# Kernel optimization log

Measured on AMD Instinct MI355X. Metric: run time of the kernel, lower is better.

The kernel has to match this reference:

```python
import jax, jax.numpy as jnp
import numpy as np

L, B, Q, D = 6, 2, 300, 256  # levels, batch, num queries, embed dim


def setup_inputs() -> dict:
    key = jax.random.key(0)
    ks = jax.random.split(key, 20)
    s = 1.0 / np.sqrt(D)
    s2 = 1.0 / np.sqrt(2 * D)
    inp = {
        "hs": jax.random.normal(ks[0], (L, B, Q, D), jnp.float32),
        # per-level proj_q / proj_k (Linear(D, D) cloned L times)
        "Wq": jax.random.uniform(ks[1], (L, D, D), jnp.float32, -s, s),
        "bq": jax.random.uniform(ks[2], (L, D), jnp.float32, -s, s),
        "Wk": jax.random.uniform(ks[3], (L, D, D), jnp.float32, -s, s),
        "bk": jax.random.uniform(ks[4], (L, D), jnp.float32, -s, s),
        # final subject/object projections on hs[-1]
        "Wsub": jax.random.uniform(ks[5], (D, D), jnp.float32, -s, s),
        "bsub": jax.random.uniform(ks[6], (D,), jnp.float32, -s, s),
        "Wobj": jax.random.uniform(ks[7], (D, D), jnp.float32, -s, s),
        "bobj": jax.random.uniform(ks[8], (D,), jnp.float32, -s, s),
        # gate: Linear(2D, 1)
        "Wg": jax.random.uniform(ks[9], (2 * D, 1), jnp.float32, -s2, s2),
        "bg": jax.random.uniform(ks[10], (1,), jnp.float32, -s2, s2),
        # MLPHEAD: 2D -> D -> D -> 1
        "W1": jax.random.uniform(ks[11], (2 * D, D), jnp.float32, -s2, s2),
        "b1": jax.random.uniform(ks[12], (D,), jnp.float32, -s2, s2),
        "W2": jax.random.uniform(ks[13], (D, D), jnp.float32, -s, s),
        "b2": jax.random.uniform(ks[14], (D,), jnp.float32, -s, s),
        "W3": jax.random.uniform(ks[15], (D, 1), jnp.float32, -s, s),
        "b3": jax.random.uniform(ks[16], (1,), jnp.float32, -s, s),
    }
    return inp


def reference(hs, Wq, bq, Wk, bk, Wsub, bsub, Wobj, bobj, Wg, bg, W1, b1, W2, b2, W3, b3):
    l, b, q, d = hs.shape
    # per-level projections: [L, B, Q, D]
    Qs = jnp.einsum('lbqd,lde->lbqe', hs, Wq) + bq[:, None, None, :]
    Ks = jnp.einsum('lbqd,lde->lbqe', hs, Wk) + bk[:, None, None, :]
    # extra (L+1)-th level from final sub/obj projections of hs[-1]
    sub = hs[-1] @ Wsub + bsub  # [B, Q, D]
    obj = hs[-1] @ Wobj + bobj
    Q_all = jnp.concatenate([Qs, sub[None]], axis=0)  # [L+1, B, Q, D]
    K_all = jnp.concatenate([Ks, obj[None]], axis=0)
    # gate logit for pair (i, j) at level m = wa.q_m[i] + wb.k_m[j] + bg,
    # identical math to sigmoid(Linear(cat([q_i, k_j]))) without materializing
    # the [B, Q, Q, L+1, 2D] broadcast tensor.
    wa, wb = Wg[:d, 0], Wg[d:, 0]
    gq = jnp.einsum('lbqd,d->lbq', Q_all, wa)  # [L+1, B, Q]
    gk = jnp.einsum('lbqd,d->lbq', K_all, wb)
    gate = jax.nn.sigmoid(gq[:, :, :, None] + gk[:, :, None, :] + bg[0])  # [L+1, B, Qi, Qj]
    # gated sum over levels; query half depends on i, key half on j
    out_q = jnp.einsum('lbij,lbid->bijd', gate, Q_all)  # [B, Q, Q, D]
    out_k = jnp.einsum('lbij,lbjd->bijd', gate, K_all)
    gated = jnp.concatenate([out_q, out_k], axis=-1)  # [B, Q, Q, 2D]
    # rel predictor MLP: 2D -> D -> D -> 1
    x = jax.nn.relu(gated @ W1 + b1)
    x = jax.nn.relu(x @ W2 + b2)
    pred = (x @ W3 + b3)[..., 0]  # [B, Q, Q]
    pred_rel = jnp.broadcast_to(pred[None], (l,) + pred.shape)  # [L, B, Q, Q]
    return pred_rel
```

## Files before the change

### kernel.cpp

```cpp
#include <hip/hip_runtime.h>


typedef _Float16 half8 __attribute__((ext_vector_type(8)));
typedef float floatx4 __attribute__((ext_vector_type(4)));

#define MFMA16(a, b, c) __builtin_amdgcn_mfma_f32_16x16x32_f16((a), (b), (c), 0, 0, 0)

__global__ __launch_bounds__(256) void k_wprep(
    const float* __restrict__ Wq, const float* __restrict__ Wk,
    const float* __restrict__ Wsub, const float* __restrict__ Wobj,
    const float* __restrict__ W1, const float* __restrict__ W2,
    _Float16* __restrict__ WT)
{
    int eid = blockIdx.x * 256 + threadIdx.x;
    int mat = eid >> 13;
    int rem = eid & 8191;
    int tileid = rem >> 6;
    int lane = rem & 63;
    const float* src;
    if      (mat < 6)  src = Wq + mat * 65536;
    else if (mat < 12) src = Wk + (mat - 6) * 65536;
    else if (mat == 12) src = Wsub;
    else if (mat == 13) src = Wobj;
    else if (mat == 14) src = W1;
    else if (mat == 15) src = W1 + 65536;
    else               src = W2;
    int nb = tileid >> 3, kb = tileid & 7;
    int n = nb * 16 + (lane & 15);
    int k = kb * 32 + (lane >> 4) * 8;
    half8 h;
    #pragma unroll
    for (int j = 0; j < 8; ++j) h[j] = (_Float16)src[(k + j) * 256 + n];
    *(half8*)(WT + mat * 65536 + tileid * 512 + lane * 8) = h;
}

__global__ __launch_bounds__(256) void k_projpq(
    const float* __restrict__ hs, const _Float16* __restrict__ WT,
    const float* __restrict__ bq, const float* __restrict__ bk,
    const float* __restrict__ bsub, const float* __restrict__ bobj,
    const float* __restrict__ Wg,
    _Float16* __restrict__ PQt, _Float16* __restrict__ PKt,
    float* __restrict__ g_ws)
{
    __shared__ __align__(16) _Float16 Ah[64][264];
    __shared__ __align__(16) _Float16 X[64][264];

    int bid = blockIdx.x;
    int s = bid / 5, mt5 = bid - s * 5;
    int qk = s & 1, rr = s >> 1;
    int l = rr % 7, b = rr / 7;
    int hs_l = (l < 6) ? l : 5;
    const float* src = hs + (hs_l * 2 + b) * 76800;
    int projmat = (l < 6) ? (qk * 6 + l) : (12 + qk);
    const _Float16* WprojT = WT + projmat * 65536;
    const _Float16* W1hT   = WT + (14 + qk) * 65536;
    const float* bias = (l < 6) ? ((qk ? bk : bq) + l * 256) : (qk ? bobj : bsub);
    _Float16* dstP = qk ? PKt : PQt;
    const float* wvec = Wg + qk * 256;
    float* gdst = g_ws + qk * 4200 + (l * 2 + b) * 300;
    int m0 = mt5 * 64;

    int t = threadIdx.x, lane = t & 63, wv = t >> 6;
    int mr = lane & 15, hf = lane >> 4;

    {
        int row = t >> 2, qt = t & 3;
        int m = m0 + row; if (m > 299) m = 299;
        const float* p = src + m * 256 + qt * 64;
        #pragma unroll
        for (int i = 0; i < 16; ++i) {
            float4 v = *(const float4*)(p + 4 * i);
            _Float16* d = &Ah[row][qt * 64 + 4 * i];
            d[0] = (_Float16)v.x; d[1] = (_Float16)v.y;
            d[2] = (_Float16)v.z; d[3] = (_Float16)v.w;
        }
    }
    __syncthreads();

    floatx4 acc[4][4];
    #pragma unroll
    for (int i = 0; i < 4; ++i)
        #pragma unroll
        for (int j = 0; j < 4; ++j) acc[i][j] = floatx4{0.f, 0.f, 0.f, 0.f};
    for (int ks = 0; ks < 8; ++ks) {
        half8 afr[4];
        #pragma unroll
        for (int mt = 0; mt < 4; ++mt)
            afr[mt] = *(const half8*)&Ah[mt * 16 + mr][ks * 32 + hf * 8];
        #pragma unroll
        for (int nt = 0; nt < 4; ++nt) {
            half8 bfr = *(const half8*)(WprojT + (((wv * 4 + nt) * 8 + ks) << 9) + lane * 8);
            #pragma unroll
            for (int mt = 0; mt < 4; ++mt)
                acc[mt][nt] = MFMA16(afr[mt], bfr, acc[mt][nt]);
        }
    }

    #pragma unroll
    for (int nt = 0; nt < 4; ++nt) {
        int col = wv * 64 + nt * 16 + mr;
        float bb = bias[col];
        #pragma unroll
        for (int mt = 0; mt < 4; ++mt)
            #pragma unroll
            for (int r = 0; r < 4; ++r)
                X[mt * 16 + hf * 4 + r][col] = (_Float16)(acc[mt][nt][r] + bb);
    }
    __syncthreads();

    {
        int row = t >> 2, qt = t & 3;
        float sum = 0.f;
        #pragma unroll
        for (int i = 0; i < 64; i += 8) {
            half8 xv = *(const half8*)&X[row][qt * 64 + i];
            const float* wp = wvec + qt * 64 + i;
            float4 w0 = *(const float4*)wp;
            float4 w1 = *(const float4*)(wp + 4);
            sum += (float)xv[0] * w0.x + (float)xv[1] * w0.y
                 + (float)xv[2] * w0.z + (float)xv[3] * w0.w
                 + (float)xv[4] * w1.x + (float)xv[5] * w1.y
                 + (float)xv[6] * w1.z + (float)xv[7] * w1.w;
        }
        sum += __shfl_xor(sum, 1);
        sum += __shfl_xor(sum, 2);
        int m = m0 + row;
        if (qt == 0 && m < 300) gdst[m] = sum;
    }

    floatx4 acc2[4][4];
    #pragma unroll
    for (int i = 0; i < 4; ++i)
        #pragma unroll
        for (int j = 0; j < 4; ++j) acc2[i][j] = floatx4{0.f, 0.f, 0.f, 0.f};
    for (int ks = 0; ks < 8; ++ks) {
        half8 afr[4];
        #pragma unroll
        for (int mt = 0; mt < 4; ++mt)
            afr[mt] = *(const half8*)&X[mt * 16 + mr][ks * 32 + hf * 8];
        #pragma unroll
        for (int nt = 0; nt < 4; ++nt) {
            half8 bfr = *(const half8*)(W1hT + (((wv * 4 + nt) * 8 + ks) << 9) + lane * 8);
            #pragma unroll
            for (int mt = 0; mt < 4; ++mt)
                acc2[mt][nt] = MFMA16(afr[mt], bfr, acc2[mt][nt]);
        }
    }

    #pragma unroll
    for (int nt = 0; nt < 4; ++nt) {
        int n = wv * 64 + nt * 16 + mr;
        #pragma unroll
        for (int mt = 0; mt < 4; ++mt)
            #pragma unroll
            for (int r = 0; r < 4; ++r) {
                int m = m0 + mt * 16 + hf * 4 + r;
                if (m < 300)
                    dstP[((size_t)(b * 38 + (m >> 3)) * 256 + n) * 56 + l * 8 + (m & 7)] =
                        (_Float16)acc2[mt][nt][r];
            }
    }
}

__global__ __launch_bounds__(256, 4) void k_fused(
    const _Float16* __restrict__ PQt, const _Float16* __restrict__ PKt,
    const float* __restrict__ g_ws, const float* __restrict__ b1,
    const _Float16* __restrict__ W2T, const float* __restrict__ b2,
    const float* __restrict__ W3, const float* __restrict__ b3,
    const float* __restrict__ bg, float* __restrict__ out)
{
    union SM {
        _Float16 Pt[256][72];
        _Float16 X[64][264];
    };
    __shared__ __align__(16) SM sm;
    __shared__ float gate[7][64];

    int t = threadIdx.x, lane = t & 63, wv = t >> 6;
    int mr = lane & 15, hf = lane >> 4;
    int bid = blockIdx.x;
    int b = bid / 1444, rem = bid - b * 1444;
    int it = rem / 38, jt = rem - it * 38;
    int i0 = it * 8, j0 = jt * 8;

    float bg0 = bg[0];
    for (int task = t; task < 448; task += 256) {
        int l = task >> 6, row = task & 63;
        int i = i0 + (row >> 3); if (i > 299) i = 299;
        int j = j0 + (row & 7);  if (j > 299) j = 299;
        float z = g_ws[l * 600 + b * 300 + i] + g_ws[4200 + l * 600 + b * 300 + j] + bg0;
        gate[l][row] = 1.0f / (1.0f + expf(-z));
    }

    floatx4 acc1[4][4];
    #pragma unroll
    for (int i = 0; i < 4; ++i)
        #pragma unroll
        for (int j = 0; j < 4; ++j) acc1[i][j] = floatx4{0.f, 0.f, 0.f, 0.f};

    for (int pass = 0; pass < 2; ++pass) {
        const _Float16* src = pass ? PKt : PQt;
        int tb = pass ? jt : it;
        const _Float16* gp = src + ((size_t)(b * 38 + tb) * 256 + t) * 56;
        __syncthreads();
        #pragma unroll
        for (int l = 0; l < 7; ++l)
            *(half8*)&sm.Pt[t][l * 8] = *(const half8*)(gp + l * 8);
        *(half8*)&sm.Pt[t][56] = half8{};
        __syncthreads();

        #pragma unroll
        for (int ktl = 0; ktl < 2; ++ktl) {
            int l = ktl * 4 + hf;
            half8 afr[4];
            #pragma unroll
            for (int mt = 0; mt < 4; ++mt) {
                int r = mt * 16 + mr;
                float g = (l < 7) ? gate[l][r] : 0.f;
                _Float16 gh = (_Float16)g;
                int jstar = pass ? (r & 7) : (r >> 3);
                half8 f;
                #pragma unroll
                for (int j = 0; j < 8; ++j)
                    f[j] = (j == jstar) ? gh : (_Float16)0.f;
                afr[mt] = f;
            }
            #pragma unroll
            for (int nt = 0; nt < 4; ++nt) {
                half8 bfr = *(const half8*)&sm.Pt[wv * 64 + nt * 16 + mr][ktl * 32 + hf * 8];
                #pragma unroll
                for (int mt = 0; mt < 4; ++mt)
                    acc1[mt][nt] = MFMA16(afr[mt], bfr, acc1[mt][nt]);
            }
        }
    }
    __syncthreads();

    #pragma unroll
    for (int nt = 0; nt < 4; ++nt) {
        int col = wv * 64 + nt * 16 + mr;
        float bb = b1[col];
        #pragma unroll
        for (int mt = 0; mt < 4; ++mt)
            #pragma unroll
            for (int r = 0; r < 4; ++r) {
                float v = acc1[mt][nt][r] + bb;
                v = v > 0.f ? v : 0.f;
                sm.X[mt * 16 + hf * 4 + r][col] = (_Float16)v;
            }
    }
    __syncthreads();

    floatx4 acc2[4][4];
    #pragma unroll
    for (int i = 0; i < 4; ++i)
        #pragma unroll
        for (int j = 0; j < 4; ++j) acc2[i][j] = floatx4{0.f, 0.f, 0.f, 0.f};
    for (int s = 0; s < 8; ++s) {
        half8 afr[4];
        #pragma unroll
        for (int mt = 0; mt < 4; ++mt)
            afr[mt] = *(const half8*)&sm.X[mt * 16 + mr][s * 32 + hf * 8];
        #pragma unroll
        for (int nt = 0; nt < 4; ++nt) {
            half8 bfr = *(const half8*)(W2T + (((wv * 4 + nt) * 8 + s) << 9) + lane * 8);
            #pragma unroll
            for (int mt = 0; mt < 4; ++mt)
                acc2[mt][nt] = MFMA16(afr[mt], bfr, acc2[mt][nt]);
        }
    }
    __syncthreads();

    #pragma unroll
    for (int nt = 0; nt < 4; ++nt) {
        int col = wv * 64 + nt * 16 + mr;
        float bb = b2[col];
        #pragma unroll
        for (int mt = 0; mt < 4; ++mt)
            #pragma unroll
            for (int r = 0; r < 4; ++r) {
                float v = acc2[mt][nt][r] + bb;
                v = v > 0.f ? v : 0.f;
                sm.X[mt * 16 + hf * 4 + r][col] = (_Float16)v;
            }
    }
    __syncthreads();

    {
        int r = t >> 2, qd = t & 3;
        float sum = 0.f;
        #pragma unroll
        for (int dd = 0; dd < 64; dd += 8) {
            half8 xv = *(const half8*)&sm.X[r][qd * 64 + dd];
            float4 w0 = *(const float4*)(W3 + qd * 64 + dd);
            float4 w1 = *(const float4*)(W3 + qd * 64 + dd + 4);
            sum += (float)xv[0] * w0.x + (float)xv[1] * w0.y
                 + (float)xv[2] * w0.z + (float)xv[3] * w0.w
                 + (float)xv[4] * w1.x + (float)xv[5] * w1.y
                 + (float)xv[6] * w1.z + (float)xv[7] * w1.w;
        }
        sum += __shfl_xor(sum, 1);
        sum += __shfl_xor(sum, 2);
        if (qd == 0) {
            int i = i0 + (r >> 3), j = j0 + (r & 7);
            if (i < 300 && j < 300) {
                float pred = sum + b3[0];
                int base = b * 90000 + i * 300 + j;
                #pragma unroll
                for (int lo = 0; lo < 6; ++lo) out[lo * 180000 + base] = pred;
            }
        }
    }
}

extern "C" void kernel_launch(void* const* d_in, const int* in_sizes, int n_in,
                              void* d_out, int out_size, void* d_ws, size_t ws_size,
                              hipStream_t stream) {
    (void)in_sizes; (void)n_in; (void)out_size; (void)ws_size;
    const float* hs   = (const float*)d_in[0];
    const float* Wq   = (const float*)d_in[1];
    const float* bq   = (const float*)d_in[2];
    const float* Wk   = (const float*)d_in[3];
    const float* bk   = (const float*)d_in[4];
    const float* Wsub = (const float*)d_in[5];
    const float* bsub = (const float*)d_in[6];
    const float* Wobj = (const float*)d_in[7];
    const float* bobj = (const float*)d_in[8];
    const float* Wg   = (const float*)d_in[9];
    const float* bg   = (const float*)d_in[10];
    const float* W1   = (const float*)d_in[11];
    const float* b1   = (const float*)d_in[12];
    const float* W2   = (const float*)d_in[13];
    const float* b2   = (const float*)d_in[14];
    const float* W3   = (const float*)d_in[15];
    const float* b3   = (const float*)d_in[16];

    char* ws = (char*)d_ws;
    float* g_ws   = (float*)ws;
    _Float16* WT  = (_Float16*)(ws + 33600);
    _Float16* PQt = WT + 17 * 65536;
    _Float16* PKt = PQt + 1089536;

    k_wprep<<<544, 256, 0, stream>>>(Wq, Wk, Wsub, Wobj, W1, W2, WT);
    k_projpq<<<140, 256, 0, stream>>>(hs, WT, bq, bk, bsub, bobj, Wg,
                                      PQt, PKt, g_ws);
    k_fused<<<2888, 256, 0, stream>>>(PQt, PKt, g_ws, b1, WT + 16 * 65536,
                                      b2, W3, b3, bg, (float*)d_out);
}
```

Before: 177.5 us.

## Swap MFMA operand roles for vectorized epilogue stores and halve projection row tiles

The MFMA operands are swapped (weights/feature rows as A, activations as B), so each lane's accumulator holds four consecutive output columns. The bias+ReLU epilogues can then write half4 vectors to shared memory instead of scalar fp16 stores, and the bias is loaded as a float4. The projection kernel moves from 64-row to 32-row tiles, which doubles its grid to 280 blocks. It also transposes the result through LDS so the PQt/PKt global writes become half8 vector stores instead of scattered scalar stores. The cost is that k_projpq reloads the weight fragments for half as many rows per block.

Result: faster. 168.3 us (-5.2%).

```diff
diff --git a/kernel.cpp b/kernel.cpp
--- a/kernel.cpp
+++ b/kernel.cpp
@@ -2,6 +2,7 @@
 
 
 typedef _Float16 half8 __attribute__((ext_vector_type(8)));
+typedef _Float16 half4v __attribute__((ext_vector_type(4)));
 typedef float floatx4 __attribute__((ext_vector_type(4)));
 
 #define MFMA16(a, b, c) __builtin_amdgcn_mfma_f32_16x16x32_f16((a), (b), (c), 0, 0, 0)
@@ -42,11 +43,12 @@
     _Float16* __restrict__ PQt, _Float16* __restrict__ PKt,
     float* __restrict__ g_ws)
 {
-    __shared__ __align__(16) _Float16 Ah[64][264];
-    __shared__ __align__(16) _Float16 X[64][264];
+    __shared__ __align__(16) _Float16 Ah[32][264];
+    __shared__ __align__(16) _Float16 X[32][264];
 
     int bid = blockIdx.x;
-    int s = bid / 5, mt5 = bid - s * 5;
+    int s = bid / 10, rt = bid - s * 10;
+    int m0 = rt * 32;
     int qk = s & 1, rr = s >> 1;
     int l = rr % 7, b = rr / 7;
     int hs_l = (l < 6) ? l : 5;
@@ -58,63 +60,67 @@
     _Float16* dstP = qk ? PKt : PQt;
     const float* wvec = Wg + qk * 256;
     float* gdst = g_ws + qk * 4200 + (l * 2 + b) * 300;
-    int m0 = mt5 * 64;
 
     int t = threadIdx.x, lane = t & 63, wv = t >> 6;
     int mr = lane & 15, hf = lane >> 4;
 
     {
-        int row = t >> 2, qt = t & 3;
+        int row = t >> 3, qt = t & 7;
         int m = m0 + row; if (m > 299) m = 299;
-        const float* p = src + m * 256 + qt * 64;
-        #pragma unroll
-        for (int i = 0; i < 16; ++i) {
+        const float* p = src + m * 256 + qt * 32;
+        #pragma unroll
+        for (int i = 0; i < 8; ++i) {
             float4 v = *(const float4*)(p + 4 * i);
-            _Float16* d = &Ah[row][qt * 64 + 4 * i];
-            d[0] = (_Float16)v.x; d[1] = (_Float16)v.y;
-            d[2] = (_Float16)v.z; d[3] = (_Float16)v.w;
-        }
-    }
-    __syncthreads();
-
-    floatx4 acc[4][4];
+            half4v h;
+            h[0] = (_Float16)v.x; h[1] = (_Float16)v.y;
+            h[2] = (_Float16)v.z; h[3] = (_Float16)v.w;
+            *(half4v*)&Ah[row][qt * 32 + 4 * i] = h;
+        }
+    }
+    __syncthreads();
+
+    floatx4 acc[4][2];
     #pragma unroll
     for (int i = 0; i < 4; ++i)
         #pragma unroll
-        for (int j = 0; j < 4; ++j) acc[i][j] = floatx4{0.f, 0.f, 0.f, 0.f};
+        for (int j = 0; j < 2; ++j) acc[i][j] = floatx4{0.f, 0.f, 0.f, 0.f};
     for (int ks = 0; ks < 8; ++ks) {
-        half8 afr[4];
-        #pragma unroll
-        for (int mt = 0; mt < 4; ++mt)
-            afr[mt] = *(const half8*)&Ah[mt * 16 + mr][ks * 32 + hf * 8];
-        #pragma unroll
-        for (int nt = 0; nt < 4; ++nt) {
-            half8 bfr = *(const half8*)(WprojT + (((wv * 4 + nt) * 8 + ks) << 9) + lane * 8);
-            #pragma unroll
-            for (int mt = 0; mt < 4; ++mt)
-                acc[mt][nt] = MFMA16(afr[mt], bfr, acc[mt][nt]);
-        }
-    }
-
-    #pragma unroll
-    for (int nt = 0; nt < 4; ++nt) {
-        int col = wv * 64 + nt * 16 + mr;
-        float bb = bias[col];
-        #pragma unroll
-        for (int mt = 0; mt < 4; ++mt)
-            #pragma unroll
-            for (int r = 0; r < 4; ++r)
-                X[mt * 16 + hf * 4 + r][col] = (_Float16)(acc[mt][nt][r] + bb);
+        half8 bfr[2];
+        #pragma unroll
+        for (int nt = 0; nt < 2; ++nt)
+            bfr[nt] = *(const half8*)&Ah[nt * 16 + mr][ks * 32 + hf * 8];
+        #pragma unroll
+        for (int mt = 0; mt < 4; ++mt) {
+            half8 afr = *(const half8*)(WprojT + (((wv * 4 + mt) * 8 + ks) << 9) + lane * 8);
+            #pragma unroll
+            for (int nt = 0; nt < 2; ++nt)
+                acc[mt][nt] = MFMA16(afr, bfr[nt], acc[mt][nt]);
+        }
+    }
+
+    #pragma unroll
+    for (int mt = 0; mt < 4; ++mt) {
+        int n0 = wv * 64 + mt * 16 + hf * 4;
+        float4 bb = *(const float4*)&bias[n0];
+        float bv[4] = {bb.x, bb.y, bb.z, bb.w};
+        #pragma unroll
+        for (int nt = 0; nt < 2; ++nt) {
+            int r = nt * 16 + mr;
+            half4v h;
+            #pragma unroll
+            for (int u = 0; u < 4; ++u) h[u] = (_Float16)(acc[mt][nt][u] + bv[u]);
+            *(half4v*)&X[r][n0] = h;
+        }
     }
     __syncthreads();
 
     {
-        int row = t >> 2, qt = t & 3;
+        int row = t >> 3, qt = t & 7;
         float sum = 0.f;
         #pragma unroll
-        for (int i = 0; i < 64; i += 8) {
-            half8 xv = *(const half8*)&X[row][qt * 64 + i];
-            const float* wp = wvec + qt * 64 + i;
+        for (int i = 0; i < 32; i += 8) {
+            half8 xv = *(const half8*)&X[row][qt * 32 + i];
+            const float* wp = wvec + qt * 32 + i;
             float4 w0 = *(const float4*)wp;
             float4 w1 = *(const float4*)(wp + 4);
             sum += (float)xv[0] * w0.x + (float)xv[1] * w0.y
@@ -124,41 +130,54 @@
         }
         sum += __shfl_xor(sum, 1);
         sum += __shfl_xor(sum, 2);
+        sum += __shfl_xor(sum, 4);
         int m = m0 + row;
         if (qt == 0 && m < 300) gdst[m] = sum;
     }
 
-    floatx4 acc2[4][4];
+    floatx4 acc2[4][2];
     #pragma unroll
     for (int i = 0; i < 4; ++i)
         #pragma unroll
-        for (int j = 0; j < 4; ++j) acc2[i][j] = floatx4{0.f, 0.f, 0.f, 0.f};
+        for (int j = 0; j < 2; ++j) acc2[i][j] = floatx4{0.f, 0.f, 0.f, 0.f};
     for (int ks = 0; ks < 8; ++ks) {
-        half8 afr[4];
-        #pragma unroll
-        for (int mt = 0; mt < 4; ++mt)
-            afr[mt] = *(const half8*)&X[mt * 16 + mr][ks * 32 + hf * 8];
-        #pragma unroll
-        for (int nt = 0; nt < 4; ++nt) {
-            half8 bfr = *(const half8*)(W1hT + (((wv * 4 + nt) * 8 + ks) << 9) + lane * 8);
-            #pragma unroll
-            for (int mt = 0; mt < 4; ++mt)
-                acc2[mt][nt] = MFMA16(afr[mt], bfr, acc2[mt][nt]);
-        }
-    }
-
-    #pragma unroll
-    for (int nt = 0; nt < 4; ++nt) {
-        int n = wv * 64 + nt * 16 + mr;
-        #pragma unroll
-        for (int mt = 0; mt < 4; ++mt)
-            #pragma unroll
-            for (int r = 0; r < 4; ++r) {
-                int m = m0 + mt * 16 + hf * 4 + r;
-                if (m < 300)
-                    dstP[((size_t)(b * 38 + (m >> 3)) * 256 + n) * 56 + l * 8 + (m & 7)] =
-                        (_Float16)acc2[mt][nt][r];
-            }
+        half8 bfr[2];
+        #pragma unroll
+        for (int nt = 0; nt < 2; ++nt)
+            bfr[nt] = *(const half8*)&X[nt * 16 + mr][ks * 32 + hf * 8];
+        #pragma unroll
+        for (int mt = 0; mt < 4; ++mt) {
+            half8 afr = *(const half8*)(W1hT + (((wv * 4 + mt) * 8 + ks) << 9) + lane * 8);
+            #pragma unroll
+            for (int nt = 0; nt < 2; ++nt)
+                acc2[mt][nt] = MFMA16(afr, bfr[nt], acc2[mt][nt]);
+        }
+    }
+
+    #pragma unroll
+    for (int mt = 0; mt < 4; ++mt) {
+        int n0 = wv * 64 + mt * 16 + hf * 4;
+        #pragma unroll
+        for (int nt = 0; nt < 2; ++nt) {
+            int r = nt * 16 + mr;
+            half4v h;
+            #pragma unroll
+            for (int u = 0; u < 4; ++u) h[u] = (_Float16)acc2[mt][nt][u];
+            *(half4v*)&Ah[r][n0] = h;
+        }
+    }
+    __syncthreads();
+
+    for (int z = 0; z < 4; ++z) {
+        int task = z * 256 + t;
+        int it4 = task >> 8, n = task & 255;
+        int it = rt * 4 + it4;
+        if (it < 38) {
+            half8 h;
+            #pragma unroll
+            for (int io = 0; io < 8; ++io) h[io] = Ah[it4 * 8 + io][n];
+            *(half8*)(dstP + ((size_t)(b * 38 + it) * 256 + n) * 56 + l * 8) = h;
+        }
     }
 }
 
@@ -212,10 +231,10 @@
         #pragma unroll
         for (int ktl = 0; ktl < 2; ++ktl) {
             int l = ktl * 4 + hf;
-            half8 afr[4];
-            #pragma unroll
-            for (int mt = 0; mt < 4; ++mt) {
-                int r = mt * 16 + mr;
+            half8 bfr[4];
+            #pragma unroll
+            for (int nt = 0; nt < 4; ++nt) {
+                int r = nt * 16 + mr;
                 float g = (l < 7) ? gate[l][r] : 0.f;
                 _Float16 gh = (_Float16)g;
                 int jstar = pass ? (r & 7) : (r >> 3);
@@ -223,31 +242,35 @@
                 #pragma unroll
                 for (int j = 0; j < 8; ++j)
                     f[j] = (j == jstar) ? gh : (_Float16)0.f;
-                afr[mt] = f;
-            }
-            #pragma unroll
-            for (int nt = 0; nt < 4; ++nt) {
-                half8 bfr = *(const half8*)&sm.Pt[wv * 64 + nt * 16 + mr][ktl * 32 + hf * 8];
+                bfr[nt] = f;
+            }
+            #pragma unroll
+            for (int mt = 0; mt < 4; ++mt) {
+                half8 afr = *(const half8*)&sm.Pt[wv * 64 + mt * 16 + mr][ktl * 32 + hf * 8];
                 #pragma unroll
-                for (int mt = 0; mt < 4; ++mt)
-                    acc1[mt][nt] = MFMA16(afr[mt], bfr, acc1[mt][nt]);
-            }
-        }
-    }
-    __syncthreads();
-
-    #pragma unroll
-    for (int nt = 0; nt < 4; ++nt) {
-        int col = wv * 64 + nt * 16 + mr;
-        float bb = b1[col];
-        #pragma unroll
-        for (int mt = 0; mt < 4; ++mt)
-            #pragma unroll
-            for (int r = 0; r < 4; ++r) {
-                float v = acc1[mt][nt][r] + bb;
-                v = v > 0.f ? v : 0.f;
-                sm.X[mt * 16 + hf * 4 + r][col] = (_Float16)v;
-            }
+                for (int nt = 0; nt < 4; ++nt)
+                    acc1[mt][nt] = MFMA16(afr, bfr[nt], acc1[mt][nt]);
+            }
+        }
+    }
+    __syncthreads();
+
+    #pragma unroll
+    for (int mt = 0; mt < 4; ++mt) {
+        int n0 = wv * 64 + mt * 16 + hf * 4;
+        float4 bb = *(const float4*)&b1[n0];
+        float bv[4] = {bb.x, bb.y, bb.z, bb.w};
+        #pragma unroll
+        for (int nt = 0; nt < 4; ++nt) {
+            int r = nt * 16 + mr;
+            half4v h;
+            #pragma unroll
+            for (int u = 0; u < 4; ++u) {
+                float v = acc1[mt][nt][u] + bv[u];
+                h[u] = (_Float16)(v > 0.f ? v : 0.f);
+            }
+            *(half4v*)&sm.X[r][n0] = h;
+        }
     }
     __syncthreads();
 
@@ -257,32 +280,36 @@
         #pragma unroll
         for (int j = 0; j < 4; ++j) acc2[i][j] = floatx4{0.f, 0.f, 0.f, 0.f};
     for (int s = 0; s < 8; ++s) {
-        half8 afr[4];
-        #pragma unroll
-        for (int mt = 0; mt < 4; ++mt)
-            afr[mt] = *(const half8*)&sm.X[mt * 16 + mr][s * 32 + hf * 8];
+        half8 bfr[4];
+        #pragma unroll
+        for (int nt = 0; nt < 4; ++nt)
+            bfr[nt] = *(const half8*)&sm.X[nt * 16 + mr][s * 32 + hf * 8];
+        #pragma unroll
+        for (int mt = 0; mt < 4; ++mt) {
+            half8 afr = *(const half8*)(W2T + (((wv * 4 + mt) * 8 + s) << 9) + lane * 8);
+            #pragma unroll
+            for (int nt = 0; nt < 4; ++nt)
+                acc2[mt][nt] = MFMA16(afr, bfr[nt], acc2[mt][nt]);
+        }
+    }
+    __syncthreads();
+
+    #pragma unroll
+    for (int mt = 0; mt < 4; ++mt) {
+        int n0 = wv * 64 + mt * 16 + hf * 4;
+        float4 bb = *(const float4*)&b2[n0];
+        float bv[4] = {bb.x, bb.y, bb.z, bb.w};
         #pragma unroll
         for (int nt = 0; nt < 4; ++nt) {
-            half8 bfr = *(const half8*)(W2T + (((wv * 4 + nt) * 8 + s) << 9) + lane * 8);
-            #pragma unroll
-            for (int mt = 0; mt < 4; ++mt)
-                acc2[mt][nt] = MFMA16(afr[mt], bfr, acc2[mt][nt]);
-        }
-    }
-    __syncthreads();
-
-    #pragma unroll
-    for (int nt = 0; nt < 4; ++nt) {
-        int col = wv * 64 + nt * 16 + mr;
-        float bb = b2[col];
-        #pragma unroll
-        for (int mt = 0; mt < 4; ++mt)
-            #pragma unroll
-            for (int r = 0; r < 4; ++r) {
-                float v = acc2[mt][nt][r] + bb;
-                v = v > 0.f ? v : 0.f;
-                sm.X[mt * 16 + hf * 4 + r][col] = (_Float16)v;
-            }
+            int r = nt * 16 + mr;
+            half4v h;
+            #pragma unroll
+            for (int u = 0; u < 4; ++u) {
+                float v = acc2[mt][nt][u] + bv[u];
+                h[u] = (_Float16)(v > 0.f ? v : 0.f);
+            }
+            *(half4v*)&sm.X[r][n0] = h;
+        }
     }
     __syncthreads();
 
@@ -342,7 +369,7 @@
     _Float16* PKt = PQt + 1089536;
 
     k_wprep<<<544, 256, 0, stream>>>(Wq, Wk, Wsub, Wobj, W1, W2, WT);
-    k_projpq<<<140, 256, 0, stream>>>(hs, WT, bq, bk, bsub, bobj, Wg,
+    k_projpq<<<280, 256, 0, stream>>>(hs, WT, bq, bk, bsub, bobj, Wg,
                                       PQt, PKt, g_ws);
     k_fused<<<2888, 256, 0, stream>>>(PQt, PKt, g_ws, b1, WT + 16 * 65536,
                                       b2, W3, b3, bg, (float*)d_out);
```
